# Kernel tuning notes

Hardware: AMD Instinct MI355X
Metric: run time of the kernel (lower is better)

## Reference

```python
import jax, jax.numpy as jnp
import numpy as np

B, C, H, W = 8, 256, 64, 64
HEADS, R, TOPK_FRAC = 8, 4, 0.25
DIM = C // HEADS
SCALE = DIM ** -0.5


def setup_inputs() -> dict:
    key = jax.random.key(0)
    ks = jax.random.split(key, 8)
    s = 0.05
    return {
        "x": jax.random.normal(ks[0], (B, C, H, W), jnp.float32),
        "w_q": jax.random.normal(ks[1], (C, C), jnp.float32) * s,
        "w_k": jax.random.normal(ks[2], (C, C), jnp.float32) * s,
        "w_v": jax.random.normal(ks[3], (C, C), jnp.float32) * s,
        "w_ck": jax.random.normal(ks[4], (C, R, R), jnp.float32) * s,  # depthwise kxk
        "w_cv": jax.random.normal(ks[5], (C, R, R), jnp.float32) * s,
        "w_out": jax.random.normal(ks[6], (C, C), jnp.float32) * s,
        "b_out": jax.random.normal(ks[7], (C,), jnp.float32) * s,
    }


def _conv1x1(x, w):
    # x: [B,C,H,W], w: [O,C]
    return jnp.einsum('bchw,oc->bohw', x, w)


def _depthwise_pool(x, w):
    # depthwise conv, kernel=stride=R -> non-overlapping blocks
    b, c, h, wd = x.shape
    blocks = x.reshape(b, c, h // R, R, wd // R, R)
    return jnp.einsum('bcirjs,crs->bcij', blocks, w)


def reference(x, w_q, w_k, w_v, w_ck, w_cv, w_out, b_out):
    N = H * W
    q = _conv1x1(x, w_q)
    k = _conv1x1(x, w_k)
    v = _conv1x1(x, w_v)
    k_s = _depthwise_pool(k, w_ck)   # [B,C,H/R,W/R]
    v_s = _depthwise_pool(v, w_cv)
    n = k_s.shape[2] * k_s.shape[3]

    BH = B * HEADS
    q = q.reshape(B, HEADS, DIM, N).reshape(BH, DIM, N)
    k = k_s.reshape(B, HEADS, DIM, n).reshape(BH, DIM, n)
    v = v_s.reshape(B, HEADS, DIM, n).reshape(BH, DIM, n)

    # stage 1: full queries vs compressed keys
    attn = jax.nn.softmax(jnp.einsum('bdi,bdj->bij', q, k) * SCALE, axis=-1)
    token_score = attn.sum(axis=1)                     # [BH, n]
    top_k = max(1, int(n * TOPK_FRAC))
    _, idx = jax.lax.top_k(token_score, top_k)         # [BH, top_k]

    idx_exp = jnp.broadcast_to(idx[:, None, :], (BH, DIM, top_k))
    k_top = jnp.take_along_axis(k, idx_exp, axis=2)    # [BH, DIM, top_k]
    v_top = jnp.take_along_axis(v, idx_exp, axis=2)

    # stage 2: attend only to selected compressed tokens
    attn_full = jax.nn.softmax(jnp.einsum('bdi,bdj->bij', q, k_top) * SCALE, axis=-1)
    out = jnp.einsum('bij,bdj->bdi', attn_full, v_top)  # [BH, DIM, N]
    out = out.reshape(B, HEADS, DIM, N).reshape(B, C, H, W)
    return _conv1x1(out, w_out) + b_out[None, :, None, None]
```

## Files before the change

kernel.cpp:

```cpp
#include <hip/hip_runtime.h>

#define Bq 8
#define Cq 256
#define Hq 64
#define Wq 64
#define Nq 4096
#define HEADSq 8
#define DIMq 32
#define NCq 256
#define TOPKq 64
#define BHq 64
#define SCALEq 0.17677669529663687f

typedef short bf16x8 __attribute__((ext_vector_type(8)));
typedef float f32x16 __attribute__((ext_vector_type(16)));

__device__ __forceinline__ uint32_t f2bf_hi(float f) {
  uint32_t u = __float_as_uint(f);
  return (u + 0x7FFFu + ((u >> 16) & 1u)) >> 16;
}

__device__ __forceinline__ void split8(const float* v, uint4& hv, uint4& lv) {
  uint32_t h[8], l[8];
#pragma unroll
  for (int j = 0; j < 8; ++j) {
    uint32_t hb = f2bf_hi(v[j]);
    float rest = v[j] - __uint_as_float(hb << 16);
    h[j] = hb;
    l[j] = __float_as_uint(rest) >> 16;
  }
  hv = make_uint4(h[0] | (h[1] << 16), h[2] | (h[3] << 16),
                  h[4] | (h[5] << 16), h[6] | (h[7] << 16));
  lv = make_uint4(l[0] | (l[1] << 16), l[2] | (l[3] << 16),
                  l[4] | (l[5] << 16), l[6] | (l[7] << 16));
}


__global__ __launch_bounds__(256) void prep_w(
    const float* __restrict__ wq, const float* __restrict__ wk,
    const float* __restrict__ wv, const float* __restrict__ wo,
    char* __restrict__ wt) {
  const int oblk = blockIdx.x, s = blockIdx.y, mat = blockIdx.z;
  const float* w = mat == 0 ? wq : mat == 1 ? wk : mat == 2 ? wv : wo;
  const int t = threadIdx.x;
  const int o = t & 63, g = t >> 6;
  float v[8];
  const float* src = w + (size_t)(oblk * 64 + o) * Cq + s * 32 + g * 8;
#pragma unroll
  for (int j = 0; j < 8; ++j) v[j] = src[j];
  uint4 hv, lv;
  split8(v, hv, lv);
  size_t base = ((size_t)((mat * 4 + oblk) * 8 + s)) * 8192;
  int off = ((o >> 5) * 2 + (g >> 1)) * 1024 + ((o & 31) + 32 * (g & 1)) * 16;
  *(uint4*)(wt + base + off) = hv;
  *(uint4*)(wt + base + 4096 + off) = lv;
}

__global__ __launch_bounds__(128) void prep_w32(
    const float* __restrict__ wq, const float* __restrict__ wk,
    const float* __restrict__ wv, char* __restrict__ wt32) {
  const int oblk = blockIdx.x, s = blockIdx.y, mat = blockIdx.z;
  const float* w = mat == 0 ? wq : mat == 1 ? wk : wv;
  const int t = threadIdx.x;
  const int o = t & 31, g = t >> 5;
  float v[8];
  const float* src = w + (size_t)(oblk * 32 + o) * Cq + s * 32 + g * 8;
#pragma unroll
  for (int j = 0; j < 8; ++j) v[j] = src[j];
  uint4 hv, lv;
  split8(v, hv, lv);
  size_t base = ((size_t)((mat * 8 + oblk) * 8 + s)) * 4096;
  int off = (g >> 1) * 1024 + (o + 32 * (g & 1)) * 16;
  *(uint4*)(wt32 + base + off) = hv;
  *(uint4*)(wt32 + base + 2048 + off) = lv;
}

__global__ __launch_bounds__(256) void prep_x(
    const float* __restrict__ x, char* __restrict__ xt) {
  const int n64 = blockIdx.x, s = blockIdx.y, b = blockIdx.z;
  const int t = threadIdx.x;
  __shared__ float xf[32][64];
  const float* xb = x + ((size_t)(b * Cq + s * 32)) * Nq + n64 * 64;
#pragma unroll
  for (int ii = 0; ii < 2; ++ii) {
    int e = t + ii * 256;
    int cl = e >> 4, n4 = (e & 15) * 4;
    *(float4*)&xf[cl][n4] = *(const float4*)&xb[(size_t)cl * Nq + n4];
  }
  __syncthreads();
  int n = t & 63, g = t >> 6;
  float v[8];
#pragma unroll
  for (int j = 0; j < 8; ++j) v[j] = xf[g * 8 + j][n];
  uint4 hv, lv;
  split8(v, hv, lv);
  char* dst = xt + ((size_t)((b * 8 + s) * 128 + n64 * 2 + (n >> 5))) * 4096;
  int off = (g >> 1) * 1024 + ((n & 31) + 32 * (g & 1)) * 16;
  *(uint4*)(dst + off) = hv;
  *(uint4*)(dst + 2048 + off) = lv;
}

__global__ __launch_bounds__(256) void qkv_fused(
    const char* __restrict__ wt32, const char* __restrict__ xt,
    const float* __restrict__ wck, const float* __restrict__ wcv,
    char* __restrict__ qimg, float* __restrict__ ksc, float* __restrict__ vsc) {
  const int i = blockIdx.x, oblk = blockIdx.y, b = blockIdx.z;
  const int t = threadIdx.x, l = t & 63, wid = t >> 6;
  __shared__ __align__(16) short wimg[3][2][1024];
  __shared__ float qf[32][256];
  __shared__ float pp[4][2][32][16];
  __shared__ float wpool[2][32][16];

  for (int u = t; u < 1024; u += 256) {
    int m = u >> 9, c = (u >> 4) & 31, e = u & 15;
    wpool[m][c][e] = (m ? wcv : wck)[(oblk * 32 + c) * 16 + e];
  }

  f32x16 acc[3][2];
#pragma unroll
  for (int m = 0; m < 3; ++m)
#pragma unroll
    for (int nt = 0; nt < 2; ++nt)
#pragma unroll
      for (int r = 0; r < 16; ++r) acc[m][nt][r] = 0.f;

  for (int s = 0; s < 8; ++s) {
    __syncthreads();
#pragma unroll
    for (int u = 0; u < 3; ++u) {
      int e = t + u * 256;
      int m = e >> 8, r = e & 255;
      ((uint4*)&wimg[m][0][0])[r] =
          ((const uint4*)(wt32 + ((size_t)((m * 8 + oblk) * 8 + s)) * 4096))[r];
    }
    __syncthreads();
    bf16x8 xh[2][2], xl[2][2];
#pragma unroll
    for (int nt = 0; nt < 2; ++nt) {
      const char* xb = xt + ((size_t)((b * 8 + s) * 128 + i * 8 + wid * 2 + nt)) * 4096;
#pragma unroll
      for (int kh = 0; kh < 2; ++kh) {
        int off = kh * 1024 + l * 16;
        xh[nt][kh] = *(const bf16x8*)(xb + off);
        xl[nt][kh] = *(const bf16x8*)(xb + 2048 + off);
      }
    }
#pragma unroll
    for (int m = 0; m < 3; ++m)
#pragma unroll
      for (int kh = 0; kh < 2; ++kh) {
        int off = kh * 1024 + l * 16;
        bf16x8 ah = *(const bf16x8*)((const char*)&wimg[m][0][0] + off);
        bf16x8 al = *(const bf16x8*)((const char*)&wimg[m][1][0] + off);
#pragma unroll
        for (int nt = 0; nt < 2; ++nt) {
          acc[m][nt] = __builtin_amdgcn_mfma_f32_32x32x16_bf16(ah, xh[nt][kh], acc[m][nt], 0, 0, 0);
          acc[m][nt] = __builtin_amdgcn_mfma_f32_32x32x16_bf16(ah, xl[nt][kh], acc[m][nt], 0, 0, 0);
          acc[m][nt] = __builtin_amdgcn_mfma_f32_32x32x16_bf16(al, xh[nt][kh], acc[m][nt], 0, 0, 0);
        }
      }
  }

#pragma unroll
  for (int nt = 0; nt < 2; ++nt)
#pragma unroll
    for (int r = 0; r < 16; ++r) {
      int c_l = (r & 3) + 8 * (r >> 2) + 4 * (l >> 5);
      qf[c_l][wid * 64 + nt * 32 + (l & 31)] = acc[0][nt][r];
    }
#pragma unroll
  for (int m = 1; m <= 2; ++m)
#pragma unroll
    for (int nt = 0; nt < 2; ++nt)
#pragma unroll
      for (int r = 0; r < 16; ++r) {
        int c_l = (r & 3) + 8 * (r >> 2) + 4 * (l >> 5);
        float sv = acc[m][nt][r] * wpool[m - 1][c_l][wid * 4 + (l & 3)];
        float t0 = sv + __shfl_xor(sv, 1);
        float s4 = t0 + __shfl_xor(t0, 2);
        if ((l & 3) == 0)
          pp[wid][m - 1][c_l][nt * 8 + ((l & 31) >> 2)] = s4;
      }
  __syncthreads();
  const int bh = b * 8 + oblk;
  {
    int row = t & 63, dg = t >> 6;
#pragma unroll
    for (int rb = 0; rb < 4; ++rb) {
      float v[8];
#pragma unroll
      for (int j = 0; j < 8; ++j) v[j] = qf[dg * 8 + j][rb * 64 + row];
      uint4 hv, lv;
      split8(v, hv, lv);
      char* qb = qimg + ((size_t)(bh * 64 + i * 4 + rb)) * 8192;
      int off = ((row >> 5) * 2 + (dg >> 1)) * 1024 + ((row & 31) + 32 * (dg & 1)) * 16;
      *(uint4*)(qb + off) = hv;
      *(uint4*)(qb + 4096 + off) = lv;
    }
  }
  {
    int c = t >> 3, jj = t & 7;
#pragma unroll
    for (int m = 0; m < 2; ++m)
#pragma unroll
      for (int rep = 0; rep < 2; ++rep) {
        int j = jj + rep * 8;
        float v = pp[0][m][c][j] + pp[1][m][c][j] + pp[2][m][c][j] + pp[3][m][c][j];
        float* dst = m ? vsc : ksc;
        dst[((size_t)b * Cq + oblk * 32 + c) * NCq + i * 16 + j] = v;
      }
  }
}

__global__ __launch_bounds__(256, 2) void stage1_mfma(
    const char* __restrict__ qim, const float* __restrict__ ks,
    float* __restrict__ part) {
  const int bh = blockIdx.y, b = bh >> 3, h = bh & 7;
  const int t = threadIdx.x, l = t & 63, wid = t >> 6;
  __shared__ __align__(16) short kimg[2][4][2048];
  __shared__ __align__(16) float xf[32][128];
  __shared__ float sc[4][256];

  const float* kb = ks + ((size_t)b * Cq + h * DIMq) * NCq;
#pragma unroll
  for (int half = 0; half < 2; ++half) {
    __syncthreads();
#pragma unroll
    for (int ii = 0; ii < 4; ++ii) {
      int row = (t >> 5) + ii * 8, c4 = (t & 31) * 4;
      *(float4*)&xf[row][c4] =
          *(const float4*)&kb[(size_t)row * NCq + half * 128 + c4];
    }
    __syncthreads();
#pragma unroll
    for (int ii = 0; ii < 2; ++ii) {
      int e = t + ii * 256;
      int n = e & 127, g = e >> 7;
      float v[8];
#pragma unroll
      for (int j = 0; j < 8; ++j) v[j] = xf[g * 8 + j][n];
      uint4 hv, lv;
      split8(v, hv, lv);
      int img = half * 2 + (n >> 6), row = n & 63;
      int off = ((row >> 5) * 2 + (g >> 1)) * 1024 +
                ((row & 31) + 32 * (g & 1)) * 16;
      *(uint4*)((char*)&kimg[0][img][0] + off) = hv;
      *(uint4*)((char*)&kimg[1][img][0] + off) = lv;
    }
  }
  __syncthreads();

  float scoreacc[8];
#pragma unroll
  for (int g = 0; g < 8; ++g) scoreacc[g] = 0.f;

  for (int step = 0; step < 4; ++step) {
    const int rowblk = blockIdx.x * 8 + step * 2 + (wid >> 1);
    const char* qb = qim + ((size_t)(bh * 64 + rowblk)) * 8192;
    bf16x8 ah[2], al[2];
#pragma unroll
    for (int kh = 0; kh < 2; ++kh) {
      int off = ((wid & 1) * 2 + kh) * 1024 + l * 16;
      ah[kh] = *(const bf16x8*)(qb + off);
      al[kh] = *(const bf16x8*)(qb + 4096 + off);
    }
    f32x16 acc[8];
#pragma unroll
    for (int g = 0; g < 8; ++g)
#pragma unroll
      for (int r = 0; r < 16; ++r) acc[g][r] = 0.f;
#pragma unroll
    for (int img = 0; img < 4; ++img)
#pragma unroll
      for (int nb = 0; nb < 2; ++nb) {
        const int g = img * 2 + nb;
#pragma unroll
        for (int kh = 0; kh < 2; ++kh) {
          int off = (nb * 2 + kh) * 1024 + l * 16;
          bf16x8 bh = *(const bf16x8*)((const char*)&kimg[0][img][0] + off);
          bf16x8 bl = *(const bf16x8*)((const char*)&kimg[1][img][0] + off);
          acc[g] = __builtin_amdgcn_mfma_f32_32x32x16_bf16(ah[kh], bh, acc[g], 0, 0, 0);
          acc[g] = __builtin_amdgcn_mfma_f32_32x32x16_bf16(ah[kh], bl, acc[g], 0, 0, 0);
          acc[g] = __builtin_amdgcn_mfma_f32_32x32x16_bf16(al[kh], bh, acc[g], 0, 0, 0);
        }
      }
    float mx[16], sm[16];
#pragma unroll
    for (int r = 0; r < 16; ++r) {
      float m = acc[0][r];
#pragma unroll
      for (int g = 1; g < 8; ++g) m = fmaxf(m, acc[g][r]);
      mx[r] = m;
    }
#pragma unroll
    for (int off = 1; off < 32; off <<= 1)
#pragma unroll
      for (int r = 0; r < 16; ++r) mx[r] = fmaxf(mx[r], __shfl_xor(mx[r], off));
#pragma unroll
    for (int r = 0; r < 16; ++r) sm[r] = 0.f;
#pragma unroll
    for (int g = 0; g < 8; ++g)
#pragma unroll
      for (int r = 0; r < 16; ++r) {
        float e = __expf((acc[g][r] - mx[r]) * SCALEq);
        acc[g][r] = e;
        sm[r] += e;
      }
#pragma unroll
    for (int off = 1; off < 32; off <<= 1)
#pragma unroll
      for (int r = 0; r < 16; ++r) sm[r] += __shfl_xor(sm[r], off);
#pragma unroll
    for (int r = 0; r < 16; ++r) sm[r] = 1.0f / sm[r];
#pragma unroll
    for (int g = 0; g < 8; ++g) {
      float tp = 0.f;
#pragma unroll
      for (int r = 0; r < 16; ++r) tp += acc[g][r] * sm[r];
      tp += __shfl_xor(tp, 32);
      scoreacc[g] += tp;
    }
  }
  if (l < 32) {
#pragma unroll
    for (int g = 0; g < 8; ++g) sc[wid][g * 32 + l] = scoreacc[g];
  }
  __syncthreads();
  {
    float v = sc[0][t] + sc[1][t] + sc[2][t] + sc[3][t];
    part[((size_t)bh * 8 + blockIdx.x) * NCq + t] = v;
  }
}

__global__ __launch_bounds__(256) void reduce_scores(
    const float* __restrict__ part, float* __restrict__ score) {
  int bh = blockIdx.x, t = threadIdx.x;
  float s = 0.f;
#pragma unroll
  for (int c = 0; c < 8; ++c) s += part[((size_t)bh * 8 + c) * NCq + t];
  score[bh * NCq + t] = s;
}

__global__ __launch_bounds__(256) void topk_sel(
    const float* __restrict__ score, int* __restrict__ idx) {
  int bh = blockIdx.x, t = threadIdx.x;
  __shared__ float s[NCq];
  s[t] = score[bh * NCq + t];
  __syncthreads();
  float st = s[t];
  int rank = 0;
  for (int j = 0; j < NCq; ++j) {
    float sj = s[j];
    rank += (sj > st) || (sj == st && j < t);
  }
  if (rank < TOPKq) idx[bh * TOPKq + rank] = t;
}

__global__ __launch_bounds__(256, 2) void stage2_mfma(
    const char* __restrict__ qim, const float* __restrict__ ks,
    const float* __restrict__ vs, const int* __restrict__ idx,
    char* __restrict__ at) {
  const int bh = blockIdx.y, b = bh >> 3, h = bh & 7;
  const int t = threadIdx.x, l = t & 63, wid = t >> 6;
  __shared__ __align__(16) short kimg[2][2048];
  __shared__ __align__(16) short vimg[2][2][1024];
  __shared__ float pbuf[128][66];
  __shared__ int ibs[64];

  const float* ksb = ks + ((size_t)b * Cq + h * DIMq) * NCq;
  const float* vsb = vs + ((size_t)b * Cq + h * DIMq) * NCq;
  if (t < 64) ibs[t] = idx[bh * TOPKq + t];
  __syncthreads();

  {
    int tok = t & 63, dg = t >> 6;
    int ti = ibs[tok];
    float v[8];
#pragma unroll
    for (int j = 0; j < 8; ++j) v[j] = ksb[(size_t)(dg * 8 + j) * NCq + ti];
    uint4 hv, lv;
    split8(v, hv, lv);
    int off = ((tok >> 5) * 2 + (dg >> 1)) * 1024 + ((tok & 31) + 32 * (dg & 1)) * 16;
    *(uint4*)((char*)&kimg[0][0] + off) = hv;
    *(uint4*)((char*)&kimg[1][0] + off) = lv;
  }
  {
    int d = l & 31, tko = l >> 5, img = (t >> 6) >> 1, kreg = (t >> 6) & 1;
    float v[8];
#pragma unroll
    for (int j = 0; j < 8; ++j) {
      int tok = img * 32 + kreg * 16 + tko * 8 + j;
      v[j] = vsb[(size_t)d * NCq + ibs[tok]];
    }
    uint4 hv, lv;
    split8(v, hv, lv);
    int off = kreg * 1024 + (d + 32 * tko) * 16;
    *(uint4*)((char*)&vimg[0][img][0] + off) = hv;
    *(uint4*)((char*)&vimg[1][img][0] + off) = lv;
  }
  __syncthreads();

  f32x16 pacc[2];
#pragma unroll
  for (int g = 0; g < 2; ++g)
#pragma unroll
    for (int r = 0; r < 16; ++r) pacc[g][r] = 0.f;
  {
    const char* qb = qim + ((size_t)(bh * 64 + blockIdx.x * 2 + (wid >> 1))) * 8192;
    bf16x8 ah[2], al[2];
#pragma unroll
    for (int kd = 0; kd < 2; ++kd) {
      int off = ((wid & 1) * 2 + kd) * 1024 + l * 16;
      ah[kd] = *(const bf16x8*)(qb + off);
      al[kd] = *(const bf16x8*)(qb + 4096 + off);
    }
#pragma unroll
    for (int g = 0; g < 2; ++g)
#pragma unroll
      for (int kd = 0; kd < 2; ++kd) {
        int off = (g * 2 + kd) * 1024 + l * 16;
        bf16x8 bh = *(const bf16x8*)((const char*)&kimg[0][0] + off);
        bf16x8 bl = *(const bf16x8*)((const char*)&kimg[1][0] + off);
        pacc[g] = __builtin_amdgcn_mfma_f32_32x32x16_bf16(ah[kd], bh, pacc[g], 0, 0, 0);
        pacc[g] = __builtin_amdgcn_mfma_f32_32x32x16_bf16(ah[kd], bl, pacc[g], 0, 0, 0);
        pacc[g] = __builtin_amdgcn_mfma_f32_32x32x16_bf16(al[kd], bh, pacc[g], 0, 0, 0);
      }
  }
  {
    float mx[16], sm[16];
#pragma unroll
    for (int r = 0; r < 16; ++r) mx[r] = fmaxf(pacc[0][r], pacc[1][r]);
#pragma unroll
    for (int off = 1; off < 32; off <<= 1)
#pragma unroll
      for (int r = 0; r < 16; ++r) mx[r] = fmaxf(mx[r], __shfl_xor(mx[r], off));
#pragma unroll
    for (int r = 0; r < 16; ++r) {
      float e0 = __expf((pacc[0][r] - mx[r]) * SCALEq);
      float e1 = __expf((pacc[1][r] - mx[r]) * SCALEq);
      pacc[0][r] = e0; pacc[1][r] = e1;
      sm[r] = e0 + e1;
    }
#pragma unroll
    for (int off = 1; off < 32; off <<= 1)
#pragma unroll
      for (int r = 0; r < 16; ++r) sm[r] += __shfl_xor(sm[r], off);
#pragma unroll
    for (int r = 0; r < 16; ++r) sm[r] = 1.0f / sm[r];
#pragma unroll
    for (int g = 0; g < 2; ++g)
#pragma unroll
      for (int r = 0; r < 16; ++r) {
        int qrow = wid * 32 + (r & 3) + 8 * (r >> 2) + 4 * (l >> 5);
        pbuf[qrow][g * 32 + (l & 31)] = pacc[g][r] * sm[r];
      }
  }
  __syncthreads();
  f32x16 oacc;
#pragma unroll
  for (int r = 0; r < 16; ++r) oacc[r] = 0.f;
#pragma unroll
  for (int ks4 = 0; ks4 < 4; ++ks4) {
    const float* pa = &pbuf[wid * 32 + (l & 31)][ks4 * 16 + (l >> 5) * 8];
    float v[8];
#pragma unroll
    for (int j = 0; j < 8; ++j) v[j] = pa[j];
    uint4 hv, lv;
    split8(v, hv, lv);
    bf16x8 pah = *(const bf16x8*)&hv, pal = *(const bf16x8*)&lv;
    int off = (ks4 & 1) * 1024 + l * 16;
    bf16x8 bh = *(const bf16x8*)((const char*)&vimg[0][ks4 >> 1][0] + off);
    bf16x8 bl = *(const bf16x8*)((const char*)&vimg[1][ks4 >> 1][0] + off);
    oacc = __builtin_amdgcn_mfma_f32_32x32x16_bf16(pah, bh, oacc, 0, 0, 0);
    oacc = __builtin_amdgcn_mfma_f32_32x32x16_bf16(pah, bl, oacc, 0, 0, 0);
    oacc = __builtin_amdgcn_mfma_f32_32x32x16_bf16(pal, bh, oacc, 0, 0, 0);
  }
#pragma unroll
  for (int r = 0; r < 16; ++r) {
    int qrow = wid * 32 + (r & 3) + 8 * (r >> 2) + 4 * (l >> 5);
    pbuf[qrow][l & 31] = oacc[r];
  }
  __syncthreads();
#pragma unroll
  for (int ii = 0; ii < 2; ++ii) {
    int slot = t + ii * 256;
    int row = slot >> 2, dg = slot & 3;
    float v[8];
#pragma unroll
    for (int j = 0; j < 8; ++j) v[j] = pbuf[row][dg * 8 + j];
    uint4 hv, lv;
    split8(v, hv, lv);
    int nb = blockIdx.x * 2 + (row >> 6), nloc = row & 63;
    size_t base = ((size_t)((b * 64 + nb) * 8 + h)) * 8192;
    int off = ((nloc >> 5) * 2 + (dg >> 1)) * 1024 +
              ((nloc & 31) + 32 * (dg & 1)) * 16;
    *(uint4*)(at + base + off) = hv;
    *(uint4*)(at + base + 4096 + off) = lv;
  }
}

__global__ __launch_bounds__(256) void out_mfma(
    const char* __restrict__ at, const char* __restrict__ wt,
    const float* __restrict__ bo, float* __restrict__ y) {
  const int b = blockIdx.z, oblk = blockIdx.y, nblk = blockIdx.x;
  const int o0 = oblk * 64, n0 = nblk * 64;
  const int t = threadIdx.x, l = t & 63, wid = t >> 6;
  const int ob = wid >> 1, nbw = wid & 1;
  __shared__ __align__(16) short wimg[2][2048];
  __shared__ __align__(16) short ximg[2][2048];
  __shared__ float bs[64];
  if (t < 64) bs[t] = bo[o0 + t];
  f32x16 acc;
#pragma unroll
  for (int i = 0; i < 16; ++i) acc[i] = 0.f;

  for (int s = 0; s < 8; ++s) {
    __syncthreads();
    {
      const uint4* srcw = (const uint4*)(wt + ((size_t)((12 + oblk) * 8 + s)) * 8192);
      const uint4* srcx = (const uint4*)(at + ((size_t)((b * 64 + nblk) * 8 + s)) * 8192);
#pragma unroll
      for (int i = 0; i < 2; ++i) {
        ((uint4*)&wimg[0][0])[t + i * 256] = srcw[t + i * 256];
        ((uint4*)&ximg[0][0])[t + i * 256] = srcx[t + i * 256];
      }
    }
    __syncthreads();
#pragma unroll
    for (int kh = 0; kh < 2; ++kh) {
      int offa = (ob * 2 + kh) * 1024 + l * 16;
      int offb = (nbw * 2 + kh) * 1024 + l * 16;
      bf16x8 ah = *(const bf16x8*)((const char*)&wimg[0][0] + offa);
      bf16x8 al = *(const bf16x8*)((const char*)&wimg[1][0] + offa);
      bf16x8 bh = *(const bf16x8*)((const char*)&ximg[0][0] + offb);
      bf16x8 bl = *(const bf16x8*)((const char*)&ximg[1][0] + offb);
      acc = __builtin_amdgcn_mfma_f32_32x32x16_bf16(ah, bh, acc, 0, 0, 0);
      acc = __builtin_amdgcn_mfma_f32_32x32x16_bf16(ah, bl, acc, 0, 0, 0);
      acc = __builtin_amdgcn_mfma_f32_32x32x16_bf16(al, bh, acc, 0, 0, 0);
    }
  }
#pragma unroll
  for (int r = 0; r < 16; ++r) {
    int ol = ob * 32 + (r & 3) + 8 * (r >> 2) + 4 * (l >> 5);
    y[((size_t)(b * Cq + o0 + ol)) * Nq + n0 + nbw * 32 + (l & 31)] = acc[r] + bs[ol];
  }
}

extern "C" void kernel_launch(void* const* d_in, const int* in_sizes, int n_in,
                              void* d_out, int out_size, void* d_ws, size_t ws_size,
                              hipStream_t stream) {
  const float* x   = (const float*)d_in[0];
  const float* wq  = (const float*)d_in[1];
  const float* wk  = (const float*)d_in[2];
  const float* wv  = (const float*)d_in[3];
  const float* wck = (const float*)d_in[4];
  const float* wcv = (const float*)d_in[5];
  const float* wo  = (const float*)d_in[6];
  const float* bo  = (const float*)d_in[7];
  float* out = (float*)d_out;

  char* wsb = (char*)d_ws;
  char*  qimg = wsb;
  char*  xt   = wsb + (size_t)33554432;
  char*  at   = xt;
  char*  wt   = wsb + (size_t)67108864;
  char*  wt32 = wsb + (size_t)68157440;
  float* ksc  = (float*)(wsb + (size_t)68943872);
  float* vsc  = ksc + (size_t)Bq * Cq * NCq;
  float* part = vsc + (size_t)Bq * Cq * NCq;
  float* score = part + (size_t)BHq * 8 * NCq;
  int*   idx  = (int*)(score + (size_t)BHq * NCq);

  prep_w<<<dim3(4, 8, 4), 256, 0, stream>>>(wq, wk, wv, wo, wt);
  prep_w32<<<dim3(8, 8, 3), 128, 0, stream>>>(wq, wk, wv, wt32);
  prep_x<<<dim3(64, 8, 8), 256, 0, stream>>>(x, xt);
  qkv_fused<<<dim3(16, 8, 8), 256, 0, stream>>>(wt32, xt, wck, wcv, qimg, ksc, vsc);
  stage1_mfma<<<dim3(8, BHq), 256, 0, stream>>>(qimg, ksc, part);
  reduce_scores<<<dim3(BHq), 256, 0, stream>>>(part, score);
  topk_sel<<<dim3(BHq), 256, 0, stream>>>(score, idx);
  stage2_mfma<<<dim3(32, BHq), 256, 0, stream>>>(qimg, ksc, vsc, idx, at);
  out_mfma<<<dim3(64, 4, 8), 256, 0, stream>>>(at, wt, bo, out);
}
```

Baseline: 200.3 us.

## Emit bf16 split key images from qkv kernel and simplify stage1 loading

The qkv projection kernel now also writes the pooled keys as pre-split hi/lo bf16 MFMA images into a new workspace buffer. Stage1 then copies those images straight into LDS instead of re-reading fp32 keys, transposing and splitting them in every block. Stage1 also doubles its grid (16 chunks of 2 steps), prefetches the next query fragment, and drops the two-blocks-per-CU launch bound. Stage2 hoists its query loads before the key/value staging. The cost is a larger partial-score buffer and reduction, plus redundant key image loads across more blocks.

```diff
diff --git a/kernel.cpp b/kernel.cpp
--- a/kernel.cpp
+++ b/kernel.cpp
@@ -103,7 +103,8 @@
 __global__ __launch_bounds__(256) void qkv_fused(
     const char* __restrict__ wt32, const char* __restrict__ xt,
     const float* __restrict__ wck, const float* __restrict__ wcv,
-    char* __restrict__ qimg, float* __restrict__ ksc, float* __restrict__ vsc) {
+    char* __restrict__ qimg, float* __restrict__ ksc, float* __restrict__ vsc,
+    char* __restrict__ kim) {
   const int i = blockIdx.x, oblk = blockIdx.y, b = blockIdx.z;
   const int t = threadIdx.x, l = t & 63, wid = t >> 6;
   __shared__ __align__(16) short wimg[3][2][1024];
@@ -198,6 +199,8 @@
       *(uint4*)(qb + 4096 + off) = lv;
     }
   }
+  float* kpool = &wpool[0][0][0];
+  float* vpool = &wpool[1][0][0];
   {
     int c = t >> 3, jj = t & 7;
 #pragma unroll
@@ -206,84 +209,89 @@
       for (int rep = 0; rep < 2; ++rep) {
         int j = jj + rep * 8;
         float v = pp[0][m][c][j] + pp[1][m][c][j] + pp[2][m][c][j] + pp[3][m][c][j];
+        (m ? vpool : kpool)[c * 16 + j] = v;
         float* dst = m ? vsc : ksc;
         dst[((size_t)b * Cq + oblk * 32 + c) * NCq + i * 16 + j] = v;
       }
   }
-}
-
-__global__ __launch_bounds__(256, 2) void stage1_mfma(
-    const char* __restrict__ qim, const float* __restrict__ ks,
+  __syncthreads();
+  if (t < 64) {
+    int tok = t >> 2, g = t & 3;
+    int img = i >> 2, row = (i & 3) * 16 + tok;
+    float v[8];
+#pragma unroll
+    for (int j = 0; j < 8; ++j) v[j] = kpool[(g * 8 + j) * 16 + tok];
+    uint4 hv, lv;
+    split8(v, hv, lv);
+    char* kb = kim + ((size_t)(bh * 4 + img)) * 8192;
+    int off = ((row >> 5) * 2 + (g >> 1)) * 1024 + ((row & 31) + 32 * (g & 1)) * 16;
+    *(uint4*)(kb + off) = hv;
+    *(uint4*)(kb + 4096 + off) = lv;
+  }
+}
+
+__global__ __launch_bounds__(256) void stage1_mfma(
+    const char* __restrict__ qim, const char* __restrict__ kim,
     float* __restrict__ part) {
-  const int bh = blockIdx.y, b = bh >> 3, h = bh & 7;
+  const int bh = blockIdx.y, chunk = blockIdx.x;
   const int t = threadIdx.x, l = t & 63, wid = t >> 6;
-  __shared__ __align__(16) short kimg[2][4][2048];
-  __shared__ __align__(16) float xf[32][128];
+  __shared__ __align__(16) char kimgL[32768];
   __shared__ float sc[4][256];
 
-  const float* kb = ks + ((size_t)b * Cq + h * DIMq) * NCq;
-#pragma unroll
-  for (int half = 0; half < 2; ++half) {
-    __syncthreads();
-#pragma unroll
-    for (int ii = 0; ii < 4; ++ii) {
-      int row = (t >> 5) + ii * 8, c4 = (t & 31) * 4;
-      *(float4*)&xf[row][c4] =
-          *(const float4*)&kb[(size_t)row * NCq + half * 128 + c4];
-    }
-    __syncthreads();
-#pragma unroll
-    for (int ii = 0; ii < 2; ++ii) {
-      int e = t + ii * 256;
-      int n = e & 127, g = e >> 7;
-      float v[8];
-#pragma unroll
-      for (int j = 0; j < 8; ++j) v[j] = xf[g * 8 + j][n];
-      uint4 hv, lv;
-      split8(v, hv, lv);
-      int img = half * 2 + (n >> 6), row = n & 63;
-      int off = ((row >> 5) * 2 + (g >> 1)) * 1024 +
-                ((row & 31) + 32 * (g & 1)) * 16;
-      *(uint4*)((char*)&kimg[0][img][0] + off) = hv;
-      *(uint4*)((char*)&kimg[1][img][0] + off) = lv;
-    }
-  }
-  __syncthreads();
-
-  float scoreacc[8];
-#pragma unroll
-  for (int g = 0; g < 8; ++g) scoreacc[g] = 0.f;
-
-  for (int step = 0; step < 4; ++step) {
-    const int rowblk = blockIdx.x * 8 + step * 2 + (wid >> 1);
-    const char* qb = qim + ((size_t)(bh * 64 + rowblk)) * 8192;
-    bf16x8 ah[2], al[2];
+  {
+    const uint4* src = (const uint4*)(kim + (size_t)bh * 32768);
+#pragma unroll
+    for (int ii = 0; ii < 8; ++ii)
+      ((uint4*)kimgL)[t + ii * 256] = src[t + ii * 256];
+  }
+  bf16x8 ah[2], al[2], nah[2], nal[2];
+  {
+    const char* qb = qim + ((size_t)(bh * 64 + chunk * 4 + (wid >> 1))) * 8192;
 #pragma unroll
     for (int kh = 0; kh < 2; ++kh) {
       int off = ((wid & 1) * 2 + kh) * 1024 + l * 16;
       ah[kh] = *(const bf16x8*)(qb + off);
       al[kh] = *(const bf16x8*)(qb + 4096 + off);
     }
+  }
+  float scoreacc[8];
+#pragma unroll
+  for (int g = 0; g < 8; ++g) scoreacc[g] = 0.f;
+  __syncthreads();
+
+#pragma unroll
+  for (int step = 0; step < 2; ++step) {
+    if (step == 0) {
+      const char* qb = qim + ((size_t)(bh * 64 + chunk * 4 + 2 + (wid >> 1))) * 8192;
+#pragma unroll
+      for (int kh = 0; kh < 2; ++kh) {
+        int off = ((wid & 1) * 2 + kh) * 1024 + l * 16;
+        nah[kh] = *(const bf16x8*)(qb + off);
+        nal[kh] = *(const bf16x8*)(qb + 4096 + off);
+      }
+    }
     f32x16 acc[8];
 #pragma unroll
     for (int g = 0; g < 8; ++g)
 #pragma unroll
       for (int r = 0; r < 16; ++r) acc[g][r] = 0.f;
 #pragma unroll
-    for (int img = 0; img < 4; ++img)
+    for (int img = 0; img < 4; ++img) {
+      const char* kb = kimgL + img * 8192;
 #pragma unroll
       for (int nb = 0; nb < 2; ++nb) {
         const int g = img * 2 + nb;
 #pragma unroll
         for (int kh = 0; kh < 2; ++kh) {
           int off = (nb * 2 + kh) * 1024 + l * 16;
-          bf16x8 bh = *(const bf16x8*)((const char*)&kimg[0][img][0] + off);
-          bf16x8 bl = *(const bf16x8*)((const char*)&kimg[1][img][0] + off);
-          acc[g] = __builtin_amdgcn_mfma_f32_32x32x16_bf16(ah[kh], bh, acc[g], 0, 0, 0);
-          acc[g] = __builtin_amdgcn_mfma_f32_32x32x16_bf16(ah[kh], bl, acc[g], 0, 0, 0);
-          acc[g] = __builtin_amdgcn_mfma_f32_32x32x16_bf16(al[kh], bh, acc[g], 0, 0, 0);
+          bf16x8 bhf = *(const bf16x8*)(kb + off);
+          bf16x8 blf = *(const bf16x8*)(kb + 4096 + off);
+          acc[g] = __builtin_amdgcn_mfma_f32_32x32x16_bf16(ah[kh], bhf, acc[g], 0, 0, 0);
+          acc[g] = __builtin_amdgcn_mfma_f32_32x32x16_bf16(ah[kh], blf, acc[g], 0, 0, 0);
+          acc[g] = __builtin_amdgcn_mfma_f32_32x32x16_bf16(al[kh], bhf, acc[g], 0, 0, 0);
         }
       }
+    }
     float mx[16], sm[16];
 #pragma unroll
     for (int r = 0; r < 16; ++r) {
@@ -320,6 +328,7 @@
       tp += __shfl_xor(tp, 32);
       scoreacc[g] += tp;
     }
+    ah[0] = nah[0]; ah[1] = nah[1]; al[0] = nal[0]; al[1] = nal[1];
   }
   if (l < 32) {
 #pragma unroll
@@ -328,7 +337,7 @@
   __syncthreads();
   {
     float v = sc[0][t] + sc[1][t] + sc[2][t] + sc[3][t];
-    part[((size_t)bh * 8 + blockIdx.x) * NCq + t] = v;
+    part[((size_t)bh * 16 + chunk) * NCq + t] = v;
   }
 }
 
@@ -337,7 +346,7 @@
   int bh = blockIdx.x, t = threadIdx.x;
   float s = 0.f;
 #pragma unroll
-  for (int c = 0; c < 8; ++c) s += part[((size_t)bh * 8 + c) * NCq + t];
+  for (int c = 0; c < 16; ++c) s += part[((size_t)bh * 16 + c) * NCq + t];
   score[bh * NCq + t] = s;
 }
 
@@ -367,6 +376,16 @@
   __shared__ float pbuf[128][66];
   __shared__ int ibs[64];
 
+  bf16x8 ah[2], al[2];
+  {
+    const char* qb = qim + ((size_t)(bh * 64 + blockIdx.x * 2 + (wid >> 1))) * 8192;
+#pragma unroll
+    for (int kd = 0; kd < 2; ++kd) {
+      int off = ((wid & 1) * 2 + kd) * 1024 + l * 16;
+      ah[kd] = *(const bf16x8*)(qb + off);
+      al[kd] = *(const bf16x8*)(qb + 4096 + off);
+    }
+  }
   const float* ksb = ks + ((size_t)b * Cq + h * DIMq) * NCq;
   const float* vsb = vs + ((size_t)b * Cq + h * DIMq) * NCq;
   if (t < 64) ibs[t] = idx[bh * TOPKq + t];
@@ -405,27 +424,17 @@
   for (int g = 0; g < 2; ++g)
 #pragma unroll
     for (int r = 0; r < 16; ++r) pacc[g][r] = 0.f;
-  {
-    const char* qb = qim + ((size_t)(bh * 64 + blockIdx.x * 2 + (wid >> 1))) * 8192;
-    bf16x8 ah[2], al[2];
+#pragma unroll
+  for (int g = 0; g < 2; ++g)
 #pragma unroll
     for (int kd = 0; kd < 2; ++kd) {
-      int off = ((wid & 1) * 2 + kd) * 1024 + l * 16;
-      ah[kd] = *(const bf16x8*)(qb + off);
-      al[kd] = *(const bf16x8*)(qb + 4096 + off);
-    }
-#pragma unroll
-    for (int g = 0; g < 2; ++g)
-#pragma unroll
-      for (int kd = 0; kd < 2; ++kd) {
-        int off = (g * 2 + kd) * 1024 + l * 16;
-        bf16x8 bh = *(const bf16x8*)((const char*)&kimg[0][0] + off);
-        bf16x8 bl = *(const bf16x8*)((const char*)&kimg[1][0] + off);
-        pacc[g] = __builtin_amdgcn_mfma_f32_32x32x16_bf16(ah[kd], bh, pacc[g], 0, 0, 0);
-        pacc[g] = __builtin_amdgcn_mfma_f32_32x32x16_bf16(ah[kd], bl, pacc[g], 0, 0, 0);
-        pacc[g] = __builtin_amdgcn_mfma_f32_32x32x16_bf16(al[kd], bh, pacc[g], 0, 0, 0);
-      }
-  }
+      int off = (g * 2 + kd) * 1024 + l * 16;
+      bf16x8 bhf = *(const bf16x8*)((const char*)&kimg[0][0] + off);
+      bf16x8 blf = *(const bf16x8*)((const char*)&kimg[1][0] + off);
+      pacc[g] = __builtin_amdgcn_mfma_f32_32x32x16_bf16(ah[kd], bhf, pacc[g], 0, 0, 0);
+      pacc[g] = __builtin_amdgcn_mfma_f32_32x32x16_bf16(ah[kd], blf, pacc[g], 0, 0, 0);
+      pacc[g] = __builtin_amdgcn_mfma_f32_32x32x16_bf16(al[kd], bhf, pacc[g], 0, 0, 0);
+    }
   {
     float mx[16], sm[16];
 #pragma unroll
@@ -469,11 +478,11 @@
     split8(v, hv, lv);
     bf16x8 pah = *(const bf16x8*)&hv, pal = *(const bf16x8*)&lv;
     int off = (ks4 & 1) * 1024 + l * 16;
-    bf16x8 bh = *(const bf16x8*)((const char*)&vimg[0][ks4 >> 1][0] + off);
-    bf16x8 bl = *(const bf16x8*)((const char*)&vimg[1][ks4 >> 1][0] + off);
-    oacc = __builtin_amdgcn_mfma_f32_32x32x16_bf16(pah, bh, oacc, 0, 0, 0);
-    oacc = __builtin_amdgcn_mfma_f32_32x32x16_bf16(pah, bl, oacc, 0, 0, 0);
-    oacc = __builtin_amdgcn_mfma_f32_32x32x16_bf16(pal, bh, oacc, 0, 0, 0);
+    bf16x8 bhf = *(const bf16x8*)((const char*)&vimg[0][ks4 >> 1][0] + off);
+    bf16x8 blf = *(const bf16x8*)((const char*)&vimg[1][ks4 >> 1][0] + off);
+    oacc = __builtin_amdgcn_mfma_f32_32x32x16_bf16(pah, bhf, oacc, 0, 0, 0);
+    oacc = __builtin_amdgcn_mfma_f32_32x32x16_bf16(pah, blf, oacc, 0, 0, 0);
+    oacc = __builtin_amdgcn_mfma_f32_32x32x16_bf16(pal, bhf, oacc, 0, 0, 0);
   }
 #pragma unroll
   for (int r = 0; r < 16; ++r) {
@@ -532,11 +541,11 @@
       int offb = (nbw * 2 + kh) * 1024 + l * 16;
       bf16x8 ah = *(const bf16x8*)((const char*)&wimg[0][0] + offa);
       bf16x8 al = *(const bf16x8*)((const char*)&wimg[1][0] + offa);
-      bf16x8 bh = *(const bf16x8*)((const char*)&ximg[0][0] + offb);
-      bf16x8 bl = *(const bf16x8*)((const char*)&ximg[1][0] + offb);
-      acc = __builtin_amdgcn_mfma_f32_32x32x16_bf16(ah, bh, acc, 0, 0, 0);
-      acc = __builtin_amdgcn_mfma_f32_32x32x16_bf16(ah, bl, acc, 0, 0, 0);
-      acc = __builtin_amdgcn_mfma_f32_32x32x16_bf16(al, bh, acc, 0, 0, 0);
+      bf16x8 bhf = *(const bf16x8*)((const char*)&ximg[0][0] + offb);
+      bf16x8 blf = *(const bf16x8*)((const char*)&ximg[1][0] + offb);
+      acc = __builtin_amdgcn_mfma_f32_32x32x16_bf16(ah, bhf, acc, 0, 0, 0);
+      acc = __builtin_amdgcn_mfma_f32_32x32x16_bf16(ah, blf, acc, 0, 0, 0);
+      acc = __builtin_amdgcn_mfma_f32_32x32x16_bf16(al, bhf, acc, 0, 0, 0);
     }
   }
 #pragma unroll
@@ -561,21 +570,22 @@
 
   char* wsb = (char*)d_ws;
   char*  qimg = wsb;
-  char*  xt   = wsb + (size_t)33554432;
+  char*  xt   = wsb + ((size_t)32 << 20);
   char*  at   = xt;
-  char*  wt   = wsb + (size_t)67108864;
-  char*  wt32 = wsb + (size_t)68157440;
-  float* ksc  = (float*)(wsb + (size_t)68943872);
-  float* vsc  = ksc + (size_t)Bq * Cq * NCq;
-  float* part = vsc + (size_t)Bq * Cq * NCq;
-  float* score = part + (size_t)BHq * 8 * NCq;
-  int*   idx  = (int*)(score + (size_t)BHq * NCq);
+  char*  wt   = wsb + ((size_t)64 << 20);
+  char*  wt32 = wsb + ((size_t)65 << 20);
+  char*  kim  = wsb + ((size_t)66 << 20);
+  float* ksc  = (float*)(wsb + ((size_t)68 << 20));
+  float* vsc  = (float*)(wsb + ((size_t)70 << 20));
+  float* part = (float*)(wsb + ((size_t)72 << 20));
+  float* score= (float*)(wsb + ((size_t)73 << 20));
+  int*   idx  = (int*)(wsb + ((size_t)73 << 20) + 65536);
 
   prep_w<<<dim3(4, 8, 4), 256, 0, stream>>>(wq, wk, wv, wo, wt);
   prep_w32<<<dim3(8, 8, 3), 128, 0, stream>>>(wq, wk, wv, wt32);
   prep_x<<<dim3(64, 8, 8), 256, 0, stream>>>(x, xt);
-  qkv_fused<<<dim3(16, 8, 8), 256, 0, stream>>>(wt32, xt, wck, wcv, qimg, ksc, vsc);
-  stage1_mfma<<<dim3(8, BHq), 256, 0, stream>>>(qimg, ksc, part);
+  qkv_fused<<<dim3(16, 8, 8), 256, 0, stream>>>(wt32, xt, wck, wcv, qimg, ksc, vsc, kim);
+  stage1_mfma<<<dim3(16, BHq), 256, 0, stream>>>(qimg, kim, part);
   reduce_scores<<<dim3(BHq), 256, 0, stream>>>(part, score);
   topk_sel<<<dim3(BHq), 256, 0, stream>>>(score, idx);
   stage2_mfma<<<dim3(32, BHq), 256, 0, stream>>>(qimg, ksc, vsc, idx, at);
```

Measured after the change: 184.1 us. 8.1% less time.
